# Kernel tuning notes

Hardware: AMD Instinct MI355X
Metric: run time of the kernel (lower is better)

## Reference

```python
import jax, jax.numpy as jnp
import numpy as np

B, NCAMS = 1, 6
C_FEAT = 64                     # fusion_feat_in_dim
H, W = 88, 160                  # per-camera feature map size at fusion level
VOX_SIZE = (100, 100, 20)       # (x_dim, y_dim, z_dim) voxel counts
VOX_STR = (-50.0, -50.0, -15.0)
VOX_UNIT = (1.0, 1.0, 1.5)
N_VOX = VOX_SIZE[0] * VOX_SIZE[1] * VOX_SIZE[2]
EPS = 1e-8
V_PRE = 64                      # voxel_pre_dim[0]


def make_voxel_pts(dtype):
    # [B, 4, N]; homogeneous (x, y, z, 1) points, layout [z, y, x] flattened
    xs = jnp.linspace(VOX_STR[0], VOX_STR[0] + VOX_UNIT[0] * (VOX_SIZE[0] - 1), VOX_SIZE[0], dtype=dtype)
    ys = jnp.linspace(VOX_STR[1], VOX_STR[1] + VOX_UNIT[1] * (VOX_SIZE[1] - 1), VOX_SIZE[1], dtype=dtype)
    zs = jnp.linspace(VOX_STR[2], VOX_STR[2] + VOX_UNIT[2] * (VOX_SIZE[2] - 1), VOX_SIZE[2], dtype=dtype)
    zdim, ydim, xdim = VOX_SIZE[2], VOX_SIZE[1], VOX_SIZE[0]
    gx = jnp.broadcast_to(xs[None, None, :], (zdim, ydim, xdim)).reshape(-1)
    gy = jnp.broadcast_to(ys[None, :, None], (zdim, ydim, xdim)).reshape(-1)
    gz = jnp.broadcast_to(zs[:, None, None], (zdim, ydim, xdim)).reshape(-1)
    pts = jnp.stack([gx, gy, gz, jnp.ones_like(gx)], axis=0)  # [4, N]
    return jnp.broadcast_to(pts[None], (B, 4, N_VOX))


def _gather(imgf, iy, ix, Wd):
    # imgf: [BN, C, H*W]; iy/ix: [BN, N] int32 -> [BN, C, N]
    lin = iy * Wd + ix
    return jnp.take_along_axis(imgf, lin[:, None, :], axis=2)


def bilinear_sample(img, gx, gy):
    # grid_sample(mode='bilinear', padding_mode='zeros', align_corners=True)
    BN, C, Hd, Wd = img.shape
    x = (gx + 1.0) * 0.5 * (Wd - 1)
    y = (gy + 1.0) * 0.5 * (Hd - 1)
    x0 = jnp.floor(x); y0 = jnp.floor(y)
    wx1 = x - x0; wx0 = 1.0 - wx1
    wy1 = y - y0; wy0 = 1.0 - wy1
    imgf = img.reshape(BN, C, Hd * Wd)
    out = jnp.zeros((BN, C, gx.shape[1]), dtype=img.dtype)
    for xi, wxi in ((x0, wx0), (x0 + 1.0, wx1)):
        for yi, wyi in ((y0, wy0), (y0 + 1.0, wy1)):
            valid = (xi >= 0) & (xi <= Wd - 1) & (yi >= 0) & (yi <= Hd - 1)
            ii = jnp.clip(xi, 0, Wd - 1).astype(jnp.int32)
            jj = jnp.clip(yi, 0, Hd - 1).astype(jnp.int32)
            w = (wxi * wyi * valid.astype(img.dtype))[:, None, :]
            out = out + _gather(imgf, jj, ii, Wd) * w
    return out


def nearest_sample(img, gx, gy):
    # grid_sample(mode='nearest', padding_mode='zeros', align_corners=True)
    BN, C, Hd, Wd = img.shape
    x = (gx + 1.0) * 0.5 * (Wd - 1)
    y = (gy + 1.0) * 0.5 * (Hd - 1)
    xi = jnp.round(x); yi = jnp.round(y)
    valid = (xi >= 0) & (xi <= Wd - 1) & (yi >= 0) & (yi <= Hd - 1)
    ii = jnp.clip(xi, 0, Wd - 1).astype(jnp.int32)
    jj = jnp.clip(yi, 0, Hd - 1).astype(jnp.int32)
    imgf = img.reshape(BN, C, Hd * Wd)
    return _gather(imgf, jj, ii, Wd) * valid[:, None, :].astype(img.dtype)


def setup_inputs() -> dict:
    key = jax.random.key(0)
    ks = jax.random.split(key, 8)
    return {
        'multi_img_feat': jax.random.normal(ks[0], (B, NCAMS, C_FEAT, H, W), jnp.float32),
        'mask': jax.random.uniform(ks[1], (B, NCAMS, 1, H, W), jnp.float32),
        'K': jax.random.normal(ks[2], (B, NCAMS, 4, 4), jnp.float32),
        'extrinsics': jax.random.normal(ks[3], (B, NCAMS, 4, 4), jnp.float32),
        'w_no': jax.random.normal(ks[4], (V_PRE, C_FEAT + 1), jnp.float32) * 0.05,
        'b_no': jax.random.normal(ks[5], (V_PRE,), jnp.float32) * 0.05,
        'w_o': jax.random.normal(ks[6], (V_PRE, 2 * (C_FEAT + 1)), jnp.float32) * 0.05,
        'b_o': jax.random.normal(ks[7], (V_PRE,), jnp.float32) * 0.05,
    }


def reference(multi_img_feat, mask, K, extrinsics, w_no, b_no, w_o, b_o):
    Bb, NC, C, Hd, Wd = multi_img_feat.shape
    dt = multi_img_feat.dtype
    vpts = make_voxel_pts(dt)                                          # [B,4,N]
    vpts_c = jnp.broadcast_to(vpts[:, None], (Bb, NC, 4, N_VOX)).reshape(Bb * NC, 4, N_VOX)
    feats = multi_img_feat.reshape(Bb * NC, C, Hd, Wd)
    masks = mask.reshape(Bb * NC, 1, Hd, Wd)                           # interp to (H,W) is identity (same size, align_corners)
    ext = extrinsics.reshape(Bb * NC, 4, 4)[:, :3, :]
    K3 = K.reshape(Bb * NC, 4, 4)[:, :3, :3]

    v_local = jnp.einsum('bij,bjn->bin', ext, vpts_c)                  # [BN,3,N]
    cam_pts = jnp.einsum('bij,bjn->bin', K3, v_local)
    pix = cam_pts[:, :2] / (cam_pts[:, 2:3] + EPS)
    pix = jnp.where(jnp.all(jnp.isfinite(pix)), pix, jnp.clip(pix, -Wd * 2.0, Wd * 2.0))
    gx = (pix[:, 0] / (Wd - 1) - 0.5) * 2.0                            # [BN,N] normalized coords
    gy = (pix[:, 1] / (Hd - 1) - 0.5) * 2.0

    feat_w = bilinear_sample(feats, gx, gy)                            # [BN,C,N]
    m_occ = nearest_sample(masks, gx, gy) > 0.5                        # [BN,1,N]
    m_depth = v_local[:, 2:3] > 0
    oob = (gx > 1) | (gx < -1) | (gy > 1) | (gy < -1)
    valid = (m_occ & m_depth & (~oob)[:, None, :]).astype(dt)          # [BN,1,N]

    feat_w = jnp.concatenate([feat_w, v_local[:, 2:3] / VOX_SIZE[0]], axis=1) * valid  # [BN,C+1,N]

    feat_w = feat_w.reshape(Bb, NC, C + 1, N_VOX)
    valid = valid.reshape(Bb, NC, 1, N_VOX)
    count = valid.sum(axis=1)                                          # [B,1,N]

    # non-overlap branch: voxels seen by exactly one camera
    no_mask = (count == 1).astype(dt)
    vox_no = feat_w.sum(axis=1) * no_mask
    vox_no = jax.nn.elu(jnp.einsum('oc,bcn->bon', w_no, vox_no) + b_no[None, :, None]) * no_mask

    # overlap branch: cams {0,3,4} vs {1,2,5}
    o_mask = (count == 2).astype(dt)
    feat1 = feat_w[:, 0] + feat_w[:, 3] + feat_w[:, 4]
    feat2 = feat_w[:, 1] + feat_w[:, 2] + feat_w[:, 5]
    vox_o = jnp.concatenate([feat1, feat2], axis=1)                    # [B,2*(C+1),N]
    vox_o = jax.nn.elu(jnp.einsum('oc,bcn->bon', w_o, vox_o) + b_o[None, :, None]) * o_mask

    return vox_no + vox_o                                              # [B, V_PRE, N]
```

## Files before the change

### kernel.cpp

```cpp
#include <hip/hip_runtime.h>
#include <cmath>

#define NC 6
#define CF 64
#define HH 88
#define WW 160
#define NPIX 14080
#define NVOX 200000
#define VPRE 64
#define VB 128
#define NTH 512
#define NWV 8

typedef unsigned int u32;

#define FEATT_BYTES  (6u * 64u * 14080u * 4u)
#define CNT_OFF      (((FEATT_BYTES) + 255u) & ~255u)
#define REC1_OFF     (CNT_OFF + 256u)
#define REC2_OFF     (REC1_OFF + (u32)NVOX * 16u)
#define WS_NEED      ((size_t)REC2_OFF + (size_t)NVOX * 32u)

__global__ __launch_bounds__(256) void transpose_feats(const float* __restrict__ in,
                                                       float* __restrict__ out,
                                                       int* __restrict__ cnt) {
    __shared__ float tile[64 * 65];
    if (cnt && blockIdx.x == 0 && threadIdx.x < 2) cnt[threadIdx.x] = 0;
    int blk = blockIdx.x;
    int c = blk / 220;
    int p0 = (blk - c * 220) * 64;
    int tid = threadIdx.x;
    int lane = tid & 63;
    int quad = tid >> 6;
    for (int r = quad; r < 64; r += 4)
        tile[r * 65 + lane] = in[(c * 64 + r) * NPIX + p0 + lane];
    __syncthreads();
    for (int r = quad; r < 64; r += 4)
        out[((c * NPIX) + p0 + r) * 64 + lane] = tile[lane * 65 + r];
}

__device__ __forceinline__ float elu1(float x) { return x > 0.0f ? x : expm1f(x); }

__device__ __forceinline__ float gather_bilin(const float* __restrict__ fsrc, int useT,
                                              int lane, int cam, float x, float y) {
    float x0f = floorf(x), y0f = floorf(y);
    float wx1 = x - x0f, wx0 = 1.0f - wx1;
    float wy1 = y - y0f, wy0 = 1.0f - wy1;
    float x1f = x0f + 1.0f, y1f = y0f + 1.0f;
    float bx0 = (x0f >= 0.0f && x0f <= 159.0f) ? 1.0f : 0.0f;
    float bx1 = (x1f >= 0.0f && x1f <= 159.0f) ? 1.0f : 0.0f;
    float by0 = (y0f >= 0.0f && y0f <= 87.0f) ? 1.0f : 0.0f;
    float by1 = (y1f >= 0.0f && y1f <= 87.0f) ? 1.0f : 0.0f;
    int ix0 = (int)fminf(fmaxf(x0f, 0.0f), 159.0f);
    int ix1 = (int)fminf(fmaxf(x1f, 0.0f), 159.0f);
    int iy0 = (int)fminf(fmaxf(y0f, 0.0f), 87.0f);
    int iy1 = (int)fminf(fmaxf(y1f, 0.0f), 87.0f);
    int A = useT ? 64 : 1;
    int Boff = useT ? (cam * NPIX * 64 + lane) : ((cam * 64 + lane) * NPIX);
    float v00 = fsrc[(iy0 * WW + ix0) * A + Boff];
    float v01 = fsrc[(iy1 * WW + ix0) * A + Boff];
    float v10 = fsrc[(iy0 * WW + ix1) * A + Boff];
    float v11 = fsrc[(iy1 * WW + ix1) * A + Boff];
    float fv;
    fv  = (wx0 * wy0 * bx0 * by0) * v00;
    fv += (wx0 * wy1 * bx0 * by1) * v01;
    fv += (wx1 * wy0 * bx1 * by0) * v10;
    fv += (wx1 * wy1 * bx1 * by1) * v11;
    return fv;
}

__global__ __launch_bounds__(256) void vox_geom(
    const float* __restrict__ mask,
    const float* __restrict__ Kg,
    const float* __restrict__ ext,
    float* __restrict__ outp,
    float4* __restrict__ rec1,
    float4* __restrict__ rec2,
    int* __restrict__ cnt)
{
    __shared__ float s_ext[72];
    __shared__ float s_K[54];
    __shared__ float4 s_r1[256];
    __shared__ float4 s_r2[512];
    __shared__ int s_c1, s_c2, s_b1, s_b2;

    int tid = threadIdx.x;
    if (tid == 0) { s_c1 = 0; s_c2 = 0; }
    if (tid >= 64 && tid < 136) {
        int i = tid - 64;
        s_ext[i] = ext[(i / 12) * 16 + (i % 12)];
    }
    if (tid >= 160 && tid < 214) {
        int i = tid - 160; int cam = i / 9; int e = i - cam * 9;
        s_K[i] = Kg[cam * 16 + (e / 3) * 4 + (e % 3)];
    }
    __syncthreads();

    int n = blockIdx.x * 256 + tid;
    if (n < NVOX) {
        #pragma clang fp contract(off)
        int xi = n % 100;
        int t = n / 100;
        int yi = t % 100;
        int zi = t / 100;
        float X = -50.0f + (float)xi;
        float Y = -50.0f + (float)yi;
        float Z = -15.0f + 1.5f * (float)zi;
        int cc = 0, cam0 = 0, cam1 = 0;
        float ax = 0.f, ay = 0.f, az = 0.f, bx = 0.f, by = 0.f, bz = 0.f;
        #pragma unroll
        for (int cam = 0; cam < NC; ++cam) {
            const float* E = s_ext + cam * 12;
            const float* Kk = s_K + cam * 9;
            float vl0 = E[0]*X + E[1]*Y + E[2]*Z + E[3];
            float vl1 = E[4]*X + E[5]*Y + E[6]*Z + E[7];
            float vl2 = E[8]*X + E[9]*Y + E[10]*Z + E[11];
            float c0 = Kk[0]*vl0 + Kk[1]*vl1 + Kk[2]*vl2;
            float c1 = Kk[3]*vl0 + Kk[4]*vl1 + Kk[5]*vl2;
            float c2 = Kk[6]*vl0 + Kk[7]*vl1 + Kk[8]*vl2;
            float pz = c2 + 1e-8f;
            float px = c0 / pz;
            float py = c1 / pz;
            float gx = (px / 159.0f - 0.5f) * 2.0f;
            float gy = (py / 87.0f - 0.5f) * 2.0f;
            float x = ((gx + 1.0f) * 0.5f) * 159.0f;
            float y = ((gy + 1.0f) * 0.5f) * 87.0f;
            float xr = rintf(x), yr = rintf(y);
            bool nv = (xr >= 0.0f) && (xr <= 159.0f) && (yr >= 0.0f) && (yr <= 87.0f);
            float mval = 0.0f;
            if (nv) mval = mask[(cam * HH + (int)yr) * WW + (int)xr];
            bool ok = (mval > 0.5f) && (vl2 > 0.0f) &&
                      !((gx > 1.0f) || (gx < -1.0f) || (gy > 1.0f) || (gy < -1.0f));
            if (ok) {
                if (cc == 0) { ax = x; ay = y; az = vl2; cam0 = cam; }
                else if (cc == 1) { bx = x; by = y; bz = vl2; cam1 = cam; }
                ++cc;
            }
        }
        if (cc == 1) {
            int s = atomicAdd(&s_c1, 1);
            s_r1[s] = make_float4(ax, ay, az, __int_as_float((n << 3) | cam0));
        } else if (cc == 2) {
            int s = atomicAdd(&s_c2, 1);
            s_r2[2 * s + 0] = make_float4(ax, ay, az, __int_as_float((n << 3) | cam0));
            s_r2[2 * s + 1] = make_float4(bx, by, bz, __int_as_float((n << 3) | cam1));
        } else {
            #pragma unroll 8
            for (int r = 0; r < 64; ++r)
                outp[(size_t)r * NVOX + n] = 0.0f;
        }
    }
    __syncthreads();
    if (tid == 0) {
        s_b1 = atomicAdd(cnt + 0, s_c1);
        s_b2 = atomicAdd(cnt + 1, s_c2);
    }
    __syncthreads();
    int c1 = s_c1, c2 = s_c2, b1 = s_b1, b2 = s_b2;
    for (int i = tid; i < c1; i += 256) rec1[b1 + i] = s_r1[i];
    for (int i = tid; i < 2 * c2; i += 256) rec2[2 * b2 + i] = s_r2[i];
}

__global__ __launch_bounds__(256) void vox_comp(
    const float* __restrict__ featT,
    const float* __restrict__ wno,
    const float* __restrict__ bno,
    const float* __restrict__ wo,
    const float* __restrict__ bo,
    float* __restrict__ outp,
    const float4* __restrict__ rec1,
    const float4* __restrict__ rec2,
    const int* __restrict__ cnt)
{
    __shared__ float s_F[65 * 66];
    __shared__ float4 s_rec[128];
    __shared__ int s_vox[64];

    int tid = threadIdx.x;
    int lane = tid & 63;
    int wv = tid >> 6;
    int wvu = __builtin_amdgcn_readfirstlane(wv);
    int obase = wvu * 16;

    int n1 = cnt[0], n2 = cnt[1];
    int T1 = (n1 + 63) >> 6;
    int T2 = (n2 + 63) >> 6;
    int TT = T1 + T2;

    for (int t = blockIdx.x; t < TT; t += gridDim.x) {
        if (t < T1) {
            int e0 = t << 6;
            int tl = min(64, n1 - e0);
            if (tid < tl) s_rec[tid] = rec1[e0 + tid];
            __syncthreads();
            for (int e = wv; e < tl; e += 4) {
                float4 r = s_rec[e];
                int meta = __float_as_int(r.w);
                int cam = meta & 7;
                float fv = gather_bilin(featT, 1, lane, cam, r.x, r.y);
                s_F[lane * 66 + e] = fv;
                if (lane == 0) { s_F[64 * 66 + e] = r.z / 100.0f; s_vox[e] = meta >> 3; }
            }
            __syncthreads();
            float acc[16];
            #pragma unroll
            for (int o = 0; o < 16; ++o) acc[o] = bno[obase + o];
            for (int cg = 0; cg < 64; cg += 4) {
                float f0 = s_F[(cg + 0) * 66 + lane];
                float f1 = s_F[(cg + 1) * 66 + lane];
                float f2 = s_F[(cg + 2) * 66 + lane];
                float f3 = s_F[(cg + 3) * 66 + lane];
                #pragma unroll
                for (int o = 0; o < 16; ++o) {
                    const float* wr = wno + (obase + o) * 65 + cg;
                    acc[o] += wr[0] * f0; acc[o] += wr[1] * f1;
                    acc[o] += wr[2] * f2; acc[o] += wr[3] * f3;
                }
            }
            {
                float fd = s_F[64 * 66 + lane];
                #pragma unroll
                for (int o = 0; o < 16; ++o) acc[o] += wno[(obase + o) * 65 + 64] * fd;
            }
            if (lane < tl) {
                size_t col = (size_t)s_vox[lane];
                #pragma unroll
                for (int o = 0; o < 16; ++o)
                    outp[(size_t)(obase + o) * NVOX + col] = elu1(acc[o]);
            }
            __syncthreads();
        } else {
            int tt = t - T1;
            int e0 = tt << 6;
            int tl = min(64, n2 - e0);
            if (tid < 2 * tl) s_rec[tid] = rec2[2 * e0 + tid];
            __syncthreads();
            for (int e = wv; e < tl; e += 4) {
                float4 r0 = s_rec[2 * e + 0];
                float4 r1 = s_rec[2 * e + 1];
                int m0 = __float_as_int(r0.w), m1 = __float_as_int(r1.w);
                int ca = m0 & 7, cb = m1 & 7;
                float fg = 0.0f, dd = 0.0f;
                if (!(ca == 1 || ca == 2 || ca == 5)) {
                    fg += gather_bilin(featT, 1, lane, ca, r0.x, r0.y);
                    dd += r0.z / 100.0f;
                }
                if (!(cb == 1 || cb == 2 || cb == 5)) {
                    fg += gather_bilin(featT, 1, lane, cb, r1.x, r1.y);
                    dd += r1.z / 100.0f;
                }
                s_F[lane * 66 + e] = fg;
                if (lane == 0) { s_F[64 * 66 + e] = dd; s_vox[e] = m0 >> 3; }
            }
            __syncthreads();
            float acc[16];
            #pragma unroll
            for (int o = 0; o < 16; ++o) acc[o] = bo[obase + o];
            for (int cg = 0; cg < 64; cg += 4) {
                float f0 = s_F[(cg + 0) * 66 + lane];
                float f1 = s_F[(cg + 1) * 66 + lane];
                float f2 = s_F[(cg + 2) * 66 + lane];
                float f3 = s_F[(cg + 3) * 66 + lane];
                #pragma unroll
                for (int o = 0; o < 16; ++o) {
                    const float* wr = wo + (obase + o) * 130 + cg;
                    acc[o] += wr[0] * f0; acc[o] += wr[1] * f1;
                    acc[o] += wr[2] * f2; acc[o] += wr[3] * f3;
                }
            }
            {
                float fd = s_F[64 * 66 + lane];
                #pragma unroll
                for (int o = 0; o < 16; ++o) acc[o] += wo[(obase + o) * 130 + 64] * fd;
            }
            __syncthreads();
            for (int e = wv; e < tl; e += 4) {
                float4 r0 = s_rec[2 * e + 0];
                float4 r1 = s_rec[2 * e + 1];
                int m0 = __float_as_int(r0.w), m1 = __float_as_int(r1.w);
                int ca = m0 & 7, cb = m1 & 7;
                float fg = 0.0f, dd = 0.0f;
                if (ca == 1 || ca == 2 || ca == 5) {
                    fg += gather_bilin(featT, 1, lane, ca, r0.x, r0.y);
                    dd += r0.z / 100.0f;
                }
                if (cb == 1 || cb == 2 || cb == 5) {
                    fg += gather_bilin(featT, 1, lane, cb, r1.x, r1.y);
                    dd += r1.z / 100.0f;
                }
                s_F[lane * 66 + e] = fg;
                if (lane == 0) s_F[64 * 66 + e] = dd;
            }
            __syncthreads();
            for (int cg = 0; cg < 64; cg += 4) {
                float f0 = s_F[(cg + 0) * 66 + lane];
                float f1 = s_F[(cg + 1) * 66 + lane];
                float f2 = s_F[(cg + 2) * 66 + lane];
                float f3 = s_F[(cg + 3) * 66 + lane];
                #pragma unroll
                for (int o = 0; o < 16; ++o) {
                    const float* wr = wo + (obase + o) * 130 + 65 + cg;
                    acc[o] += wr[0] * f0; acc[o] += wr[1] * f1;
                    acc[o] += wr[2] * f2; acc[o] += wr[3] * f3;
                }
            }
            {
                float fd = s_F[64 * 66 + lane];
                #pragma unroll
                for (int o = 0; o < 16; ++o) acc[o] += wo[(obase + o) * 130 + 129] * fd;
            }
            if (lane < tl) {
                size_t col = (size_t)s_vox[lane];
                #pragma unroll
                for (int o = 0; o < 16; ++o)
                    outp[(size_t)(obase + o) * NVOX + col] = elu1(acc[o]);
            }
            __syncthreads();
        }
    }
}

#define FMA8_STEP(W0,W1,W2,W3,W4,W5,W6,W7,CG,F0,F1,F2,F3) \
    a0 += W0[CG]*F0; a0 += W0[CG+1]*F1; a0 += W0[CG+2]*F2; a0 += W0[CG+3]*F3; \
    a1 += W1[CG]*F0; a1 += W1[CG+1]*F1; a1 += W1[CG+2]*F2; a1 += W1[CG+3]*F3; \
    a2 += W2[CG]*F0; a2 += W2[CG+1]*F1; a2 += W2[CG+2]*F2; a2 += W2[CG+3]*F3; \
    a3 += W3[CG]*F0; a3 += W3[CG+1]*F1; a3 += W3[CG+2]*F2; a3 += W3[CG+3]*F3; \
    a4 += W4[CG]*F0; a4 += W4[CG+1]*F1; a4 += W4[CG+2]*F2; a4 += W4[CG+3]*F3; \
    a5 += W5[CG]*F0; a5 += W5[CG+1]*F1; a5 += W5[CG+2]*F2; a5 += W5[CG+3]*F3; \
    a6 += W6[CG]*F0; a6 += W6[CG+1]*F1; a6 += W6[CG+2]*F2; a6 += W6[CG+3]*F3; \
    a7 += W7[CG]*F0; a7 += W7[CG+1]*F1; a7 += W7[CG+2]*F2; a7 += W7[CG+3]*F3;

#define STORE8(COL) \
    outp[(size_t)(obase + 0) * NVOX + COL] = elu1(a0); \
    outp[(size_t)(obase + 1) * NVOX + COL] = elu1(a1); \
    outp[(size_t)(obase + 2) * NVOX + COL] = elu1(a2); \
    outp[(size_t)(obase + 3) * NVOX + COL] = elu1(a3); \
    outp[(size_t)(obase + 4) * NVOX + COL] = elu1(a4); \
    outp[(size_t)(obase + 5) * NVOX + COL] = elu1(a5); \
    outp[(size_t)(obase + 6) * NVOX + COL] = elu1(a6); \
    outp[(size_t)(obase + 7) * NVOX + COL] = elu1(a7);

__global__ __launch_bounds__(NTH) void vox_fused(
    const float* __restrict__ feats,
    const float* __restrict__ featT,
    const float* __restrict__ mask,
    const float* __restrict__ Kg,
    const float* __restrict__ ext,
    const float* __restrict__ wno,
    const float* __restrict__ bno,
    const float* __restrict__ wo,
    const float* __restrict__ bo,
    float* __restrict__ outp,
    int useT)
{
    __shared__ float s_ext[72];
    __shared__ float s_K[54];
    __shared__ float s_F[65 * 66];
    __shared__ __align__(16) float4 s_rec1[VB];
    __shared__ __align__(16) float4 s_rec2[2 * VB];
    __shared__ int s_vox[64];
    __shared__ int s_n1, s_n2;

    int tid = threadIdx.x;
    int lane = tid & 63;
    int wv = tid >> 6;
    int base = blockIdx.x * VB;
    int vlim = min(VB, NVOX - base);

    if (tid == 0) { s_n1 = 0; s_n2 = 0; }
    if (tid >= 64 && tid < 136) {
        int i = tid - 64;
        s_ext[i] = ext[(i / 12) * 16 + (i % 12)];
    }
    if (tid >= 192 && tid < 246) {
        int i = tid - 192; int cam = i / 9; int e = i - cam * 9;
        s_K[i] = Kg[cam * 16 + (e / 3) * 4 + (e % 3)];
    }

    {
        int ng4 = vlim >> 2;
        for (int i = tid; i < 64 * (VB / 4); i += NTH) {
            int r = i >> 5, cg = i & ((VB / 4) - 1);
            if (cg < ng4)
                *(float4*)(outp + (size_t)r * NVOX + base + (cg << 2)) =
                    make_float4(0.f, 0.f, 0.f, 0.f);
        }
    }
    __syncthreads();

    if (tid < vlim) {
        #pragma clang fp contract(off)
        int n = base + tid;
        int xi = n % 100;
        int t = n / 100;
        int yi = t % 100;
        int zi = t / 100;
        float X = -50.0f + (float)xi;
        float Y = -50.0f + (float)yi;
        float Z = -15.0f + 1.5f * (float)zi;
        int cnt = 0, cam0 = 0, cam1 = 0;
        float ax = 0.f, ay = 0.f, az = 0.f, bx = 0.f, by = 0.f, bz = 0.f;
        #pragma unroll
        for (int cam = 0; cam < NC; ++cam) {
            const float* E = s_ext + cam * 12;
            const float* Kk = s_K + cam * 9;
            float vl0 = E[0]*X + E[1]*Y + E[2]*Z + E[3];
            float vl1 = E[4]*X + E[5]*Y + E[6]*Z + E[7];
            float vl2 = E[8]*X + E[9]*Y + E[10]*Z + E[11];
            float c0 = Kk[0]*vl0 + Kk[1]*vl1 + Kk[2]*vl2;
            float c1 = Kk[3]*vl0 + Kk[4]*vl1 + Kk[5]*vl2;
            float c2 = Kk[6]*vl0 + Kk[7]*vl1 + Kk[8]*vl2;
            float pz = c2 + 1e-8f;
            float px = c0 / pz;
            float py = c1 / pz;
            float gx = (px / 159.0f - 0.5f) * 2.0f;
            float gy = (py / 87.0f - 0.5f) * 2.0f;
            float x = ((gx + 1.0f) * 0.5f) * 159.0f;
            float y = ((gy + 1.0f) * 0.5f) * 87.0f;
            float xr = rintf(x), yr = rintf(y);
            bool nv = (xr >= 0.0f) && (xr <= 159.0f) && (yr >= 0.0f) && (yr <= 87.0f);
            float mval = 0.0f;
            if (nv) mval = mask[(cam * HH + (int)yr) * WW + (int)xr];
            bool ok = (mval > 0.5f) && (vl2 > 0.0f) &&
                      !((gx > 1.0f) || (gx < -1.0f) || (gy > 1.0f) || (gy < -1.0f));
            if (ok) {
                if (cnt == 0) { ax = x; ay = y; az = vl2; cam0 = cam; }
                else if (cnt == 1) { bx = x; by = y; bz = vl2; cam1 = cam; }
                ++cnt;
            }
        }
        if (cnt == 1) {
            int s = atomicAdd(&s_n1, 1);
            s_rec1[s] = make_float4(ax, ay, az, __int_as_float((n << 3) | cam0));
        } else if (cnt == 2) {
            int s = atomicAdd(&s_n2, 1);
            s_rec2[2 * s + 0] = make_float4(ax, ay, az, __int_as_float((n << 3) | cam0));
            s_rec2[2 * s + 1] = make_float4(bx, by, bz, __int_as_float((n << 3) | cam1));
        }
    }
    __syncthreads();

    int n1 = s_n1, n2 = s_n2;
    const float* fsrc = useT ? featT : feats;
    int wvu = __builtin_amdgcn_readfirstlane(wv);
    int obase = wvu * 8;
    const float* w0n = wno + (obase + 0) * 65;
    const float* w1n = wno + (obase + 1) * 65;
    const float* w2n = wno + (obase + 2) * 65;
    const float* w3n = wno + (obase + 3) * 65;
    const float* w4n = wno + (obase + 4) * 65;
    const float* w5n = wno + (obase + 5) * 65;
    const float* w6n = wno + (obase + 6) * 65;
    const float* w7n = wno + (obase + 7) * 65;
    const float* w0o = wo + (obase + 0) * 130;
    const float* w1o = wo + (obase + 1) * 130;
    const float* w2o = wo + (obase + 2) * 130;
    const float* w3o = wo + (obase + 3) * 130;
    const float* w4o = wo + (obase + 4) * 130;
    const float* w5o = wo + (obase + 5) * 130;
    const float* w6o = wo + (obase + 6) * 130;
    const float* w7o = wo + (obase + 7) * 130;

    for (int t0 = 0; t0 < n1; t0 += 64) {
        int tl = min(64, n1 - t0);
        for (int e = wv; e < tl; e += NWV) {
            float4 r = s_rec1[t0 + e];
            int meta = __float_as_int(r.w);
            int cam = meta & 7;
            float fv = gather_bilin(fsrc, useT, lane, cam, r.x, r.y);
            s_F[lane * 66 + e] = fv;
            if (lane == 0) { s_F[64 * 66 + e] = r.z / 100.0f; s_vox[e] = meta >> 3; }
        }
        __syncthreads();
        float a0 = bno[obase + 0], a1 = bno[obase + 1], a2 = bno[obase + 2], a3 = bno[obase + 3];
        float a4 = bno[obase + 4], a5 = bno[obase + 5], a6 = bno[obase + 6], a7 = bno[obase + 7];
        for (int cg = 0; cg < 64; cg += 4) {
            float f0 = s_F[(cg + 0) * 66 + lane];
            float f1 = s_F[(cg + 1) * 66 + lane];
            float f2 = s_F[(cg + 2) * 66 + lane];
            float f3 = s_F[(cg + 3) * 66 + lane];
            FMA8_STEP(w0n, w1n, w2n, w3n, w4n, w5n, w6n, w7n, cg, f0, f1, f2, f3)
        }
        float fd = s_F[64 * 66 + lane];
        a0 += w0n[64] * fd; a1 += w1n[64] * fd; a2 += w2n[64] * fd; a3 += w3n[64] * fd;
        a4 += w4n[64] * fd; a5 += w5n[64] * fd; a6 += w6n[64] * fd; a7 += w7n[64] * fd;
        if (lane < tl) {
            size_t col = (size_t)s_vox[lane];
            STORE8(col)
        }
        __syncthreads();
    }

    for (int t0 = 0; t0 < n2; t0 += 64) {
        int tl = min(64, n2 - t0);
        for (int e = wv; e < tl; e += NWV) {
            float4 r0 = s_rec2[2 * (t0 + e) + 0];
            float4 r1 = s_rec2[2 * (t0 + e) + 1];
            int m0 = __float_as_int(r0.w), m1 = __float_as_int(r1.w);
            int ca = m0 & 7, cb = m1 & 7;
            float fg = 0.0f, dd = 0.0f;
            if (!(ca == 1 || ca == 2 || ca == 5)) {
                fg += gather_bilin(fsrc, useT, lane, ca, r0.x, r0.y);
                dd += r0.z / 100.0f;
            }
            if (!(cb == 1 || cb == 2 || cb == 5)) {
                fg += gather_bilin(fsrc, useT, lane, cb, r1.x, r1.y);
                dd += r1.z / 100.0f;
            }
            s_F[lane * 66 + e] = fg;
            if (lane == 0) { s_F[64 * 66 + e] = dd; s_vox[e] = m0 >> 3; }
        }
        __syncthreads();
        float a0 = bo[obase + 0], a1 = bo[obase + 1], a2 = bo[obase + 2], a3 = bo[obase + 3];
        float a4 = bo[obase + 4], a5 = bo[obase + 5], a6 = bo[obase + 6], a7 = bo[obase + 7];
        for (int cg = 0; cg < 64; cg += 4) {
            float f0 = s_F[(cg + 0) * 66 + lane];
            float f1 = s_F[(cg + 1) * 66 + lane];
            float f2 = s_F[(cg + 2) * 66 + lane];
            float f3 = s_F[(cg + 3) * 66 + lane];
            FMA8_STEP(w0o, w1o, w2o, w3o, w4o, w5o, w6o, w7o, cg, f0, f1, f2, f3)
        }
        {
            float fd = s_F[64 * 66 + lane];
            a0 += w0o[64] * fd; a1 += w1o[64] * fd; a2 += w2o[64] * fd; a3 += w3o[64] * fd;
            a4 += w4o[64] * fd; a5 += w5o[64] * fd; a6 += w6o[64] * fd; a7 += w7o[64] * fd;
        }
        __syncthreads();
        for (int e = wv; e < tl; e += NWV) {
            float4 r0 = s_rec2[2 * (t0 + e) + 0];
            float4 r1 = s_rec2[2 * (t0 + e) + 1];
            int m0 = __float_as_int(r0.w), m1 = __float_as_int(r1.w);
            int ca = m0 & 7, cb = m1 & 7;
            float fg = 0.0f, dd = 0.0f;
            if (ca == 1 || ca == 2 || ca == 5) {
                fg += gather_bilin(fsrc, useT, lane, ca, r0.x, r0.y);
                dd += r0.z / 100.0f;
            }
            if (cb == 1 || cb == 2 || cb == 5) {
                fg += gather_bilin(fsrc, useT, lane, cb, r1.x, r1.y);
                dd += r1.z / 100.0f;
            }
            s_F[lane * 66 + e] = fg;
            if (lane == 0) s_F[64 * 66 + e] = dd;
        }
        __syncthreads();
        for (int cg = 0; cg < 64; cg += 4) {
            float f0 = s_F[(cg + 0) * 66 + lane];
            float f1 = s_F[(cg + 1) * 66 + lane];
            float f2 = s_F[(cg + 2) * 66 + lane];
            float f3 = s_F[(cg + 3) * 66 + lane];
            int cgo = cg + 65;
            FMA8_STEP(w0o, w1o, w2o, w3o, w4o, w5o, w6o, w7o, cgo, f0, f1, f2, f3)
        }
        {
            float fd = s_F[64 * 66 + lane];
            a0 += w0o[129] * fd; a1 += w1o[129] * fd; a2 += w2o[129] * fd; a3 += w3o[129] * fd;
            a4 += w4o[129] * fd; a5 += w5o[129] * fd; a6 += w6o[129] * fd; a7 += w7o[129] * fd;
        }
        if (lane < tl) {
            size_t col = (size_t)s_vox[lane];
            STORE8(col)
        }
        __syncthreads();
    }
}

extern "C" void kernel_launch(void* const* d_in, const int* in_sizes, int n_in,
                              void* d_out, int out_size, void* d_ws, size_t ws_size,
                              hipStream_t stream) {
    const float* feats = (const float*)d_in[0];
    const float* mask  = (const float*)d_in[1];
    const float* Kg    = (const float*)d_in[2];
    const float* ext   = (const float*)d_in[3];
    const float* wno   = (const float*)d_in[4];
    const float* bno   = (const float*)d_in[5];
    const float* wo    = (const float*)d_in[6];
    const float* bo    = (const float*)d_in[7];
    float* outp = (float*)d_out;
    float* featT = (float*)d_ws;

    if (ws_size >= WS_NEED) {
        int* cnt = (int*)((char*)d_ws + CNT_OFF);
        float4* rec1 = (float4*)((char*)d_ws + REC1_OFF);
        float4* rec2 = (float4*)((char*)d_ws + REC2_OFF);
        transpose_feats<<<NC * 220, 256, 0, stream>>>(feats, featT, cnt);
        vox_geom<<<(NVOX + 255) / 256, 256, 0, stream>>>(mask, Kg, ext, outp,
                                                         rec1, rec2, cnt);
        vox_comp<<<2048, 256, 0, stream>>>(featT, wno, bno, wo, bo, outp,
                                           rec1, rec2, cnt);
    } else {
        int useT = (ws_size >= (size_t)FEATT_BYTES) ? 1 : 0;
        if (useT) {
            transpose_feats<<<NC * 220, 256, 0, stream>>>(feats, featT, nullptr);
        }
        int nblk = (NVOX + VB - 1) / VB;
        vox_fused<<<nblk, NTH, 0, stream>>>(feats, featT, mask, Kg, ext,
                                            wno, bno, wo, bo, outp, useT);
    }
}
```

Baseline: 176.1 us.

## Zero output in a separate pass and double vox_comp block size to 512 threads

Output zeroing moves out of vox_geom's scattered per-voxel column writes into a dedicated coalesced float4 zero kernel that writes the whole output. vox_comp now runs 512 threads (8 waves), each computing 8 output channels instead of 16, which lowers register pressure and raises parallelism per tile. The per-tile gather loops are fully unrolled over 8 entries, with dummy padding records filling partial tiles. This writes the entire output twice (zero pass plus the real values) and does wasted gathers on the padded entries.

```diff
diff --git a/kernel.cpp b/kernel.cpp
--- a/kernel.cpp
+++ b/kernel.cpp
@@ -19,6 +19,13 @@
 #define REC1_OFF     (CNT_OFF + 256u)
 #define REC2_OFF     (REC1_OFF + (u32)NVOX * 16u)
 #define WS_NEED      ((size_t)REC2_OFF + (size_t)NVOX * 32u)
+
+__global__ __launch_bounds__(256) void zero_out(float4* __restrict__ p, int n4) {
+    int i = blockIdx.x * 256 + threadIdx.x;
+    int stride = gridDim.x * 256;
+    for (; i < n4; i += stride)
+        p[i] = make_float4(0.f, 0.f, 0.f, 0.f);
+}
 
 __global__ __launch_bounds__(256) void transpose_feats(const float* __restrict__ in,
                                                        float* __restrict__ out,
@@ -72,7 +79,6 @@
     const float* __restrict__ mask,
     const float* __restrict__ Kg,
     const float* __restrict__ ext,
-    float* __restrict__ outp,
     float4* __restrict__ rec1,
     float4* __restrict__ rec2,
     int* __restrict__ cnt)
@@ -143,10 +149,6 @@
             int s = atomicAdd(&s_c2, 1);
             s_r2[2 * s + 0] = make_float4(ax, ay, az, __int_as_float((n << 3) | cam0));
             s_r2[2 * s + 1] = make_float4(bx, by, bz, __int_as_float((n << 3) | cam1));
-        } else {
-            #pragma unroll 8
-            for (int r = 0; r < 64; ++r)
-                outp[(size_t)r * NVOX + n] = 0.0f;
         }
     }
     __syncthreads();
@@ -160,7 +162,7 @@
     for (int i = tid; i < 2 * c2; i += 256) rec2[2 * b2 + i] = s_r2[i];
 }
 
-__global__ __launch_bounds__(256) void vox_comp(
+__global__ __launch_bounds__(512) void vox_comp(
     const float* __restrict__ featT,
     const float* __restrict__ wno,
     const float* __restrict__ bno,
@@ -179,20 +181,24 @@
     int lane = tid & 63;
     int wv = tid >> 6;
     int wvu = __builtin_amdgcn_readfirstlane(wv);
-    int obase = wvu * 16;
+    int obase = wvu * 8;
 
     int n1 = cnt[0], n2 = cnt[1];
     int T1 = (n1 + 63) >> 6;
     int T2 = (n2 + 63) >> 6;
     int TT = T1 + T2;
+    float4 dummy = make_float4(0.f, 0.f, 0.f, __int_as_float(0));
 
     for (int t = blockIdx.x; t < TT; t += gridDim.x) {
         if (t < T1) {
             int e0 = t << 6;
             int tl = min(64, n1 - e0);
-            if (tid < tl) s_rec[tid] = rec1[e0 + tid];
-            __syncthreads();
-            for (int e = wv; e < tl; e += 4) {
+            if (tid < 64)
+                s_rec[tid] = (tid < tl) ? rec1[e0 + tid] : dummy;
+            __syncthreads();
+            #pragma unroll
+            for (int u = 0; u < 8; ++u) {
+                int e = (u << 3) | wv;
                 float4 r = s_rec[e];
                 int meta = __float_as_int(r.w);
                 int cam = meta & 7;
@@ -201,16 +207,16 @@
                 if (lane == 0) { s_F[64 * 66 + e] = r.z / 100.0f; s_vox[e] = meta >> 3; }
             }
             __syncthreads();
-            float acc[16];
+            float acc[8];
             #pragma unroll
-            for (int o = 0; o < 16; ++o) acc[o] = bno[obase + o];
+            for (int o = 0; o < 8; ++o) acc[o] = bno[obase + o];
             for (int cg = 0; cg < 64; cg += 4) {
                 float f0 = s_F[(cg + 0) * 66 + lane];
                 float f1 = s_F[(cg + 1) * 66 + lane];
                 float f2 = s_F[(cg + 2) * 66 + lane];
                 float f3 = s_F[(cg + 3) * 66 + lane];
                 #pragma unroll
-                for (int o = 0; o < 16; ++o) {
+                for (int o = 0; o < 8; ++o) {
                     const float* wr = wno + (obase + o) * 65 + cg;
                     acc[o] += wr[0] * f0; acc[o] += wr[1] * f1;
                     acc[o] += wr[2] * f2; acc[o] += wr[3] * f3;
@@ -219,12 +225,12 @@
             {
                 float fd = s_F[64 * 66 + lane];
                 #pragma unroll
-                for (int o = 0; o < 16; ++o) acc[o] += wno[(obase + o) * 65 + 64] * fd;
+                for (int o = 0; o < 8; ++o) acc[o] += wno[(obase + o) * 65 + 64] * fd;
             }
             if (lane < tl) {
                 size_t col = (size_t)s_vox[lane];
                 #pragma unroll
-                for (int o = 0; o < 16; ++o)
+                for (int o = 0; o < 8; ++o)
                     outp[(size_t)(obase + o) * NVOX + col] = elu1(acc[o]);
             }
             __syncthreads();
@@ -232,9 +238,12 @@
             int tt = t - T1;
             int e0 = tt << 6;
             int tl = min(64, n2 - e0);
-            if (tid < 2 * tl) s_rec[tid] = rec2[2 * e0 + tid];
-            __syncthreads();
-            for (int e = wv; e < tl; e += 4) {
+            if (tid < 128)
+                s_rec[tid] = (tid < 2 * tl) ? rec2[2 * e0 + tid] : dummy;
+            __syncthreads();
+            #pragma unroll
+            for (int u = 0; u < 8; ++u) {
+                int e = (u << 3) | wv;
                 float4 r0 = s_rec[2 * e + 0];
                 float4 r1 = s_rec[2 * e + 1];
                 int m0 = __float_as_int(r0.w), m1 = __float_as_int(r1.w);
@@ -252,16 +261,16 @@
                 if (lane == 0) { s_F[64 * 66 + e] = dd; s_vox[e] = m0 >> 3; }
             }
             __syncthreads();
-            float acc[16];
+            float acc[8];
             #pragma unroll
-            for (int o = 0; o < 16; ++o) acc[o] = bo[obase + o];
+            for (int o = 0; o < 8; ++o) acc[o] = bo[obase + o];
             for (int cg = 0; cg < 64; cg += 4) {
                 float f0 = s_F[(cg + 0) * 66 + lane];
                 float f1 = s_F[(cg + 1) * 66 + lane];
                 float f2 = s_F[(cg + 2) * 66 + lane];
                 float f3 = s_F[(cg + 3) * 66 + lane];
                 #pragma unroll
-                for (int o = 0; o < 16; ++o) {
+                for (int o = 0; o < 8; ++o) {
                     const float* wr = wo + (obase + o) * 130 + cg;
                     acc[o] += wr[0] * f0; acc[o] += wr[1] * f1;
                     acc[o] += wr[2] * f2; acc[o] += wr[3] * f3;
@@ -270,10 +279,12 @@
             {
                 float fd = s_F[64 * 66 + lane];
                 #pragma unroll
-                for (int o = 0; o < 16; ++o) acc[o] += wo[(obase + o) * 130 + 64] * fd;
-            }
-            __syncthreads();
-            for (int e = wv; e < tl; e += 4) {
+                for (int o = 0; o < 8; ++o) acc[o] += wo[(obase + o) * 130 + 64] * fd;
+            }
+            __syncthreads();
+            #pragma unroll
+            for (int u = 0; u < 8; ++u) {
+                int e = (u << 3) | wv;
                 float4 r0 = s_rec[2 * e + 0];
                 float4 r1 = s_rec[2 * e + 1];
                 int m0 = __float_as_int(r0.w), m1 = __float_as_int(r1.w);
@@ -297,7 +308,7 @@
                 float f2 = s_F[(cg + 2) * 66 + lane];
                 float f3 = s_F[(cg + 3) * 66 + lane];
                 #pragma unroll
-                for (int o = 0; o < 16; ++o) {
+                for (int o = 0; o < 8; ++o) {
                     const float* wr = wo + (obase + o) * 130 + 65 + cg;
                     acc[o] += wr[0] * f0; acc[o] += wr[1] * f1;
                     acc[o] += wr[2] * f2; acc[o] += wr[3] * f3;
@@ -306,12 +317,12 @@
             {
                 float fd = s_F[64 * 66 + lane];
                 #pragma unroll
-                for (int o = 0; o < 16; ++o) acc[o] += wo[(obase + o) * 130 + 129] * fd;
+                for (int o = 0; o < 8; ++o) acc[o] += wo[(obase + o) * 130 + 129] * fd;
             }
             if (lane < tl) {
                 size_t col = (size_t)s_vox[lane];
                 #pragma unroll
-                for (int o = 0; o < 16; ++o)
+                for (int o = 0; o < 8; ++o)
                     outp[(size_t)(obase + o) * NVOX + col] = elu1(acc[o]);
             }
             __syncthreads();
@@ -582,10 +593,12 @@
         int* cnt = (int*)((char*)d_ws + CNT_OFF);
         float4* rec1 = (float4*)((char*)d_ws + REC1_OFF);
         float4* rec2 = (float4*)((char*)d_ws + REC2_OFF);
+        zero_out<<<2048, 256, 0, stream>>>((float4*)d_out,
+                                           (int)((size_t)VPRE * NVOX / 4));
         transpose_feats<<<NC * 220, 256, 0, stream>>>(feats, featT, cnt);
-        vox_geom<<<(NVOX + 255) / 256, 256, 0, stream>>>(mask, Kg, ext, outp,
+        vox_geom<<<(NVOX + 255) / 256, 256, 0, stream>>>(mask, Kg, ext,
                                                          rec1, rec2, cnt);
-        vox_comp<<<2048, 256, 0, stream>>>(featT, wno, bno, wo, bo, outp,
+        vox_comp<<<2048, 512, 0, stream>>>(featT, wno, bno, wo, bo, outp,
                                            rec1, rec2, cnt);
     } else {
         int useT = (ws_size >= (size_t)FEATT_BYTES) ? 1 : 0;
```

After: 207.7 us. 1.18x slower.
